# Kernel optimization log

Measured on AMD Instinct MI355X. Metric: run time of the kernel, lower is better.

## Reference

```python
import jax, jax.numpy as jnp
import numpy as np

EPS = 1e-8  # torch.nn.CosineSimilarity default eps


def setup_inputs() -> dict:
    key = jax.random.key(0)
    H, W, C = 1024, 1024, 128
    input_image = jax.random.normal(key, (H, W, 1, C), dtype=jnp.float32)
    return {"input_image": input_image}


def reference(input_image):
    # input_image: [H, W, 1, C]; cosine similarity of each pixel with its
    # valid 3x3 neighbors (including self), summed, minus 1 (the self term).
    x = input_image[:, :, 0, :]  # [H, W, C]
    H, W, _ = x.shape
    # torch cosine: dot(a,b) / (max(||a||,eps) * max(||b||,eps))
    # = dot(a/max(||a||,eps), b/max(||b||,eps)) -> normalize once.
    norm = jnp.sqrt(jnp.sum(x * x, axis=-1, keepdims=True))
    xn = x / jnp.maximum(norm, EPS)  # [H, W, C]
    # zero-pad by 1; zero rows/cols contribute 0 == out-of-range mask in original
    xp = jnp.pad(xn, ((1, 1), (1, 1), (0, 0)))  # [H+2, W+2, C]
    sim = jnp.zeros((H, W), dtype=x.dtype)
    for k in (-1, 0, 1):
        for l in (-1, 0, 1):
            shifted = jax.lax.dynamic_slice(xp, (1 + k, 1 + l, 0), (H, W, xp.shape[-1]))
            sim = sim + jnp.einsum('hwc,hwc->hw', xn, shifted)
    return sim - 1.0
```

## Files before the change

kernel.cpp:

```cpp
#include <hip/hip_runtime.h>


#define HH 1024
#define WW 1024
#define C4 32
#define SOUT 64
#define SHALO (SOUT + 2)
#define RROWS 32
#define NT 512
#define NSTAGE ((SHALO * C4 + NT - 1) / NT)
#define OWN ((SOUT * C4) / NT)

__device__ __forceinline__ float dot4(float4 a, float4 b) {
    return fmaf(a.x, b.x, fmaf(a.y, b.y, fmaf(a.z, b.z, a.w * b.w)));
}

__device__ __forceinline__ void stage_row(const float4* __restrict__ in,
                                          int y, int x0, int t, bool need,
                                          float4 (&v)[NSTAGE]) {
#pragma unroll
    for (int i = 0; i < NSTAGE; ++i) {
        const int idx = t + i * NT;
        float4 val = make_float4(0.f, 0.f, 0.f, 0.f);
        const bool inR = (i < NSTAGE - 1) || (idx < SHALO * C4);
        if (inR) {
            const int gx = x0 - 1 + (idx >> 5);
            if (need && gx >= 0 && gx < WW) {
                val = in[(size_t)(y * WW + gx) * C4 + (idx & 31)];
            }
        }
        v[i] = val;
    }
}

__global__ __launch_bounds__(NT, 4)
void cos_sim_kernel(const float4* __restrict__ in, float* __restrict__ out) {
    __shared__ float4 xrow[2][SHALO * C4];

    const int t   = threadIdx.x;
    const int c4  = t & 31;
    const int xo0 = t >> 5;
    const int x0  = blockIdx.x * SOUT;
    const int r0  = blockIdx.y * RROWS;
    const int ylast = r0 + RROWS;

    float4 Hprev[OWN], XNprev[OWN];
    float  accP[OWN];
#pragma unroll
    for (int i = 0; i < OWN; ++i) {
        Hprev[i]  = make_float4(0.f, 0.f, 0.f, 0.f);
        XNprev[i] = make_float4(0.f, 0.f, 0.f, 0.f);
        accP[i]   = 0.f;
    }

    float4 vA[NSTAGE], vB[NSTAGE];
    stage_row(in, r0 - 1, x0, t, (r0 - 1 >= 0), vA);

    int buf = 0;
    for (int y = r0 - 1; y <= ylast; ++y) {
        const int yn = y + 1;
        stage_row(in, yn, x0, t,
                  (yn >= 0) && (yn < HH) && (yn <= ylast), vB);

#pragma unroll
        for (int i = 0; i < NSTAGE; ++i) {
            const int idx = t + i * NT;
            float s = dot4(vA[i], vA[i]);
            s += __shfl_xor(s, 1);
            s += __shfl_xor(s, 2);
            s += __shfl_xor(s, 4);
            s += __shfl_xor(s, 8);
            s += __shfl_xor(s, 16);
            const float inv = rsqrtf(fmaxf(s, 1e-16f));
            const bool inR = (i < NSTAGE - 1) || (idx < SHALO * C4);
            if (inR) {
                float4 w;
                w.x = vA[i].x * inv; w.y = vA[i].y * inv;
                w.z = vA[i].z * inv; w.w = vA[i].w * inv;
                xrow[buf][idx] = w;
            }
        }

        asm volatile("s_waitcnt lgkmcnt(0)" ::: "memory");
        __builtin_amdgcn_s_barrier();

#pragma unroll
        for (int i = 0; i < OWN; ++i) {
            const int xo = xo0 + 16 * i;
            const float4 a = xrow[buf][(xo    ) * C4 + c4];
            const float4 b = xrow[buf][(xo + 1) * C4 + c4];
            const float4 r = xrow[buf][(xo + 2) * C4 + c4];
            float4 Hc;
            Hc.x = a.x + b.x + r.x; Hc.y = a.y + b.y + r.y;
            Hc.z = a.z + b.z + r.z; Hc.w = a.w + b.w + r.w;

            float fin = accP[i] + dot4(XNprev[i], Hc);
            accP[i]   = dot4(b, Hprev[i]) + dot4(b, Hc);
            XNprev[i] = b;
            Hprev[i]  = Hc;

            if (y > r0) {
                fin += __shfl_xor(fin, 1);
                fin += __shfl_xor(fin, 2);
                fin += __shfl_xor(fin, 4);
                fin += __shfl_xor(fin, 8);
                fin += __shfl_xor(fin, 16);
                if (c4 == 0) {
                    out[(size_t)(y - 1) * WW + x0 + xo] = fin - 1.0f;
                }
            }
        }

        buf ^= 1;
#pragma unroll
        for (int i = 0; i < NSTAGE; ++i) vA[i] = vB[i];
    }
}

extern "C" void kernel_launch(void* const* d_in, const int* in_sizes, int n_in,
                              void* d_out, int out_size, void* d_ws, size_t ws_size,
                              hipStream_t stream) {
    const float4* in = (const float4*)d_in[0];
    float* out = (float*)d_out;
    dim3 grid(WW / SOUT, HH / RROWS);
    cos_sim_kernel<<<grid, NT, 0, stream>>>(in, out);
}
```

Measured before the change: 699.5 us.

## Stream rows via direct global-to-LDS loads and store per-pixel inverse norms

Replaces register-staged row prefetch with global_load_lds async copies into double-buffered shared memory. The raw values stay in LDS and only per-pixel inverse norms are stored separately, with scaling applied at use time. The tile width is halved to 32 and occupancy is raised to 6 blocks per CU. This aims to cut register pressure and improve overlap of loads with compute, at the cost of more halo re-reads and clamped dummy loads that fill the padded LDS slots.

```diff
diff --git a/kernel.cpp b/kernel.cpp
--- a/kernel.cpp
+++ b/kernel.cpp
@@ -4,38 +4,41 @@
 #define HH 1024
 #define WW 1024
 #define C4 32
-#define SOUT 64
+#define SOUT 32
 #define SHALO (SOUT + 2)
 #define RROWS 32
 #define NT 512
-#define NSTAGE ((SHALO * C4 + NT - 1) / NT)
+#define NVALID (SHALO * C4)
+#define NSTAGE 3
+#define NPAD (NSTAGE * NT)
 #define OWN ((SOUT * C4) / NT)
 
 __device__ __forceinline__ float dot4(float4 a, float4 b) {
     return fmaf(a.x, b.x, fmaf(a.y, b.y, fmaf(a.z, b.z, a.w * b.w)));
 }
 
-__device__ __forceinline__ void stage_row(const float4* __restrict__ in,
-                                          int y, int x0, int t, bool need,
-                                          float4 (&v)[NSTAGE]) {
+__device__ __forceinline__ void stage(const float4* __restrict__ in,
+                                      int y, int ymax, int x0, int t,
+                                      float4* dst ) {
+    const int yc = min(max(y, 0), ymax);
+    const size_t rowbase = (size_t)yc * WW * C4;
 #pragma unroll
     for (int i = 0; i < NSTAGE; ++i) {
-        const int idx = t + i * NT;
-        float4 val = make_float4(0.f, 0.f, 0.f, 0.f);
-        const bool inR = (i < NSTAGE - 1) || (idx < SHALO * C4);
-        if (inR) {
-            const int gx = x0 - 1 + (idx >> 5);
-            if (need && gx >= 0 && gx < WW) {
-                val = in[(size_t)(y * WW + gx) * C4 + (idx & 31)];
-            }
-        }
-        v[i] = val;
+        const int idx  = t + i * NT;
+        const int eidx = (idx < NVALID) ? idx : (idx - 2 * NT);
+        const int gx   = x0 - 1 + (eidx >> 5);
+        const int gxc  = min(max(gx, 0), WW - 1);
+        const float4* src = in + rowbase + (size_t)gxc * C4 + (eidx & 31);
+        __builtin_amdgcn_global_load_lds(
+            (const __attribute__((address_space(1))) void*)src,
+            (__attribute__((address_space(3))) void*)(dst + idx), 16, 0, 0);
     }
 }
 
-__global__ __launch_bounds__(NT, 4)
+__global__ __launch_bounds__(NT, 6)
 void cos_sim_kernel(const float4* __restrict__ in, float* __restrict__ out) {
-    __shared__ float4 xrow[2][SHALO * C4];
+    __shared__ float4 raw[2][NPAD];
+    __shared__ float  invn[2][SHALO];
 
     const int t   = threadIdx.x;
     const int c4  = t & 31;
@@ -43,6 +46,7 @@
     const int x0  = blockIdx.x * SOUT;
     const int r0  = blockIdx.y * RROWS;
     const int ylast = r0 + RROWS;
+    const int ymax  = min(ylast, HH - 1);
 
     float4 Hprev[OWN], XNprev[OWN];
     float  accP[OWN];
@@ -53,50 +57,60 @@
         accP[i]   = 0.f;
     }
 
-    float4 vA[NSTAGE], vB[NSTAGE];
-    stage_row(in, r0 - 1, x0, t, (r0 - 1 >= 0), vA);
+    stage(in, r0 - 1, ymax, x0, t, &raw[0][0]);
 
-    int buf = 0;
+    int cb = 0;
     for (int y = r0 - 1; y <= ylast; ++y) {
-        const int yn = y + 1;
-        stage_row(in, yn, x0, t,
-                  (yn >= 0) && (yn < HH) && (yn <= ylast), vB);
+        asm volatile("s_waitcnt vmcnt(0)" ::: "memory");
+        __builtin_amdgcn_s_barrier();
 
+        stage(in, y + 1, ymax, x0, t, &raw[cb ^ 1][0]);
+
+        const bool rowOK = (y >= 0) && (y < HH);
 #pragma unroll
         for (int i = 0; i < NSTAGE; ++i) {
             const int idx = t + i * NT;
-            float s = dot4(vA[i], vA[i]);
-            s += __shfl_xor(s, 1);
-            s += __shfl_xor(s, 2);
-            s += __shfl_xor(s, 4);
-            s += __shfl_xor(s, 8);
-            s += __shfl_xor(s, 16);
-            const float inv = rsqrtf(fmaxf(s, 1e-16f));
-            const bool inR = (i < NSTAGE - 1) || (idx < SHALO * C4);
-            if (inR) {
-                float4 w;
-                w.x = vA[i].x * inv; w.y = vA[i].y * inv;
-                w.z = vA[i].z * inv; w.w = vA[i].w * inv;
-                xrow[buf][idx] = w;
+            if (idx < NVALID) {
+                const int gx = x0 - 1 + (idx >> 5);
+                float4 v;
+                if (!rowOK || gx < 0 || gx >= WW) {
+                    v = make_float4(0.f, 0.f, 0.f, 0.f);
+                    raw[cb][idx] = v;
+                } else {
+                    v = raw[cb][idx];
+                }
+                float s = dot4(v, v);
+                s += __shfl_xor(s, 1);
+                s += __shfl_xor(s, 2);
+                s += __shfl_xor(s, 4);
+                s += __shfl_xor(s, 8);
+                s += __shfl_xor(s, 16);
+                if (c4 == 0) invn[cb][idx >> 5] = rsqrtf(fmaxf(s, 1e-16f));
             }
         }
-
         asm volatile("s_waitcnt lgkmcnt(0)" ::: "memory");
         __builtin_amdgcn_s_barrier();
 
 #pragma unroll
         for (int i = 0; i < OWN; ++i) {
             const int xo = xo0 + 16 * i;
-            const float4 a = xrow[buf][(xo    ) * C4 + c4];
-            const float4 b = xrow[buf][(xo + 1) * C4 + c4];
-            const float4 r = xrow[buf][(xo + 2) * C4 + c4];
+            const float4 a = raw[cb][(xo    ) * C4 + c4];
+            const float4 b = raw[cb][(xo + 1) * C4 + c4];
+            const float4 r = raw[cb][(xo + 2) * C4 + c4];
+            const float ia = invn[cb][xo];
+            const float ib = invn[cb][xo + 1];
+            const float ir = invn[cb][xo + 2];
             float4 Hc;
-            Hc.x = a.x + b.x + r.x; Hc.y = a.y + b.y + r.y;
-            Hc.z = a.z + b.z + r.z; Hc.w = a.w + b.w + r.w;
+            Hc.x = fmaf(a.x, ia, fmaf(b.x, ib, r.x * ir));
+            Hc.y = fmaf(a.y, ia, fmaf(b.y, ib, r.y * ir));
+            Hc.z = fmaf(a.z, ia, fmaf(b.z, ib, r.z * ir));
+            Hc.w = fmaf(a.w, ia, fmaf(b.w, ib, r.w * ir));
+            const float4 xb = make_float4(b.x * ib, b.y * ib,
+                                          b.z * ib, b.w * ib);
 
             float fin = accP[i] + dot4(XNprev[i], Hc);
-            accP[i]   = dot4(b, Hprev[i]) + dot4(b, Hc);
-            XNprev[i] = b;
+            accP[i]   = dot4(xb, Hprev[i]) + dot4(xb, Hc);
+            XNprev[i] = xb;
             Hprev[i]  = Hc;
 
             if (y > r0) {
@@ -110,10 +124,7 @@
                 }
             }
         }
-
-        buf ^= 1;
-#pragma unroll
-        for (int i = 0; i < NSTAGE; ++i) vA[i] = vB[i];
+        cb ^= 1;
     }
 }
 
```

Measured after the change: 752.5 us. 1.08x slower.
